# Kernel tuning notes

Hardware: AMD Instinct MI355X
Metric: run time of the kernel (lower is better)

The kernel has to match this reference:

```python
import jax, jax.numpy as jnp
import numpy as np

# Hyperparameters from init_kwargs
SIGMA = 0.01   # memristor conductance noise std
R = 1.0        # line resistance scale used in power accounting
WMAX1 = 1.0
WMAX2 = 1.0
B, C, H, W = 4, 3, 64, 64
K = 2                      # AvgPool2d kernel/stride
D1 = C * (H // K) * (W // K)   # 3072 flattened features after pooling
D2 = 2048
D3 = 1024


def setup_inputs() -> dict:
    key = jax.random.key(0)
    ks = jax.random.split(key, 4)
    x = jax.random.normal(ks[0], (B, C, H, W), jnp.float32)
    bias = jax.random.normal(ks[1], (C, H, W), jnp.float32) * 0.01
    W1 = jax.random.normal(ks[2], (D2, D1), jnp.float32) / np.float32(np.sqrt(D1))
    W2 = jax.random.normal(ks[3], (D3, D2), jnp.float32) / np.float32(np.sqrt(D2))
    g1 = jnp.float32(1.0)  # learnt_Gmax[0], initialized to Wmax[0]
    g2 = jnp.float32(1.0)  # learnt_Gmax[1]
    return {"x": x, "bias": bias, "W1": W1, "W2": W2, "g1": g1, "g2": g2}


def reference(x, bias, W1, W2, g1, g2):
    # input bias (MemSE.input_bias=True)
    x = x + bias[None]
    b = x.shape[0]
    eye2 = jnp.eye(D2, dtype=x.dtype)
    eye3 = jnp.eye(D3, dtype=x.dtype)

    # --- AvgPool2d(2,2): gamma is still empty at this point, only mean pooled ---
    x = x.reshape(b, C, H // K, K, W // K, K).mean(axis=(3, 5))
    x = x.reshape(b, -1)                        # [B, D1]

    # --- Linear 1: crossbar noise injection (gamma empty -> created here) ---
    c1 = g1 / WMAX1                             # conductance scaling G = c * W
    mu = x @ W1.T                               # [B, D2] mean propagation
    m2 = x * x                                  # E[x^2] (gamma == 0 before this layer)
    # two conductance arrays (pos/neg) each with iid noise var sigma^2, output /c
    vn1 = 2.0 * (SIGMA / c1) ** 2 * jnp.sum(m2, axis=-1)        # [B]
    gamma = vn1[:, None, None] * eye2[None]                      # [B, D2, D2]
    P_tot = (c1 / R) * jnp.einsum('oi,bi->b', jnp.abs(W1), m2)   # crossbar power

    # --- Softplus: first-order moment propagation (Jacobian = sigmoid(mu)) ---
    d = jax.nn.sigmoid(mu)                      # [B, D2]
    gamma = gamma * d[:, :, None] * d[:, None, :]
    mu = jax.nn.softplus(mu)

    # --- Linear 2: full covariance propagation W gamma W^T + noise diag ---
    c2 = g2 / WMAX2
    mu2 = mu @ W2.T                             # [B, D3]
    tmp = jnp.einsum('oi,bij->boj', W2, gamma)  # [B, D3, D2]
    gamma2 = jnp.einsum('boj,pj->bop', tmp, W2) # [B, D3, D3]
    m2b = mu * mu + jnp.diagonal(gamma, axis1=1, axis2=2)        # E[x^2]
    vn2 = 2.0 * (SIGMA / c2) ** 2 * jnp.sum(m2b, axis=-1)
    gamma2 = gamma2 + vn2[:, None, None] * eye3[None]
    P_tot = P_tot + (c2 / R) * jnp.einsum('oi,bi->b', jnp.abs(W2), m2b)

    return mu2, gamma2, P_tot
```

## Files before the change

### kernel.cpp

```cpp
#include <hip/hip_runtime.h>
#include <hip/hip_bf16.h>
#include <cstdint>

#define SIGMA 0.01f

constexpr int D1 = 3072;
constexpr int D2 = 2048;
constexpr int D3 = 1024;

typedef __bf16 bf16x8 __attribute__((ext_vector_type(8)));
typedef float f32x4 __attribute__((ext_vector_type(4)));

#define GLOAD16(gp, lp) \
  __builtin_amdgcn_global_load_lds((const __attribute__((address_space(1))) void*)(gp), \
                                   (__attribute__((address_space(3))) void*)(lp), 16, 0, 0)

__global__ void pool_kernel(const float* __restrict__ x, const float* __restrict__ bias,
                            float* __restrict__ pooled, float* __restrict__ Spart) {
  int idx = blockIdx.x * 256 + threadIdx.x;
  int b = idx / D1;
  int r = idx % D1;
  int c = r >> 10;
  int oh = (r >> 5) & 31;
  int ow = r & 31;
  int xb = ((b * 3 + c) * 64 + oh * 2) * 64 + ow * 2;
  int bb = (c * 64 + oh * 2) * 64 + ow * 2;
  float v = 0.25f * ((x[xb] + bias[bb]) + (x[xb + 1] + bias[bb + 1]) +
                     (x[xb + 64] + bias[bb + 64]) + (x[xb + 65] + bias[bb + 65]));
  pooled[idx] = v;
  float s = v * v;
  #pragma unroll
  for (int off = 32; off; off >>= 1) s += __shfl_down(s, off, 64);
  __shared__ float wsum[4];
  if ((threadIdx.x & 63) == 0) wsum[threadIdx.x >> 6] = s;
  __syncthreads();
  if (threadIdx.x == 0) Spart[blockIdx.x] = wsum[0] + wsum[1] + wsum[2] + wsum[3];
}

__global__ void lin1_kernel(const float* __restrict__ pooled, const float* __restrict__ W1,
                            const float* __restrict__ Spart, const float* __restrict__ g1p,
                            float* __restrict__ musp, float* __restrict__ dscale,
                            float* __restrict__ m2b, float* __restrict__ Pp1) {
  int o2 = blockIdx.x << 1, tid = threadIdx.x;
  const float4* w0p = (const float4*)(W1 + (size_t)o2 * D1);
  const float4* w1p = (const float4*)(W1 + (size_t)(o2 + 1) * D1);
  const float4* p4 = (const float4*)pooled;
  float a0[4] = {0,0,0,0}, q0[4] = {0,0,0,0}, a1[4] = {0,0,0,0}, q1[4] = {0,0,0,0};
  #pragma unroll
  for (int it = 0; it < 3; it++) {
    int i4 = tid + it * 256;
    float4 w0 = w0p[i4], w1 = w1p[i4];
    float x0x = fabsf(w0.x), x0y = fabsf(w0.y), x0z = fabsf(w0.z), x0w = fabsf(w0.w);
    float x1x = fabsf(w1.x), x1y = fabsf(w1.y), x1z = fabsf(w1.z), x1w = fabsf(w1.w);
    #pragma unroll
    for (int b = 0; b < 4; b++) {
      float4 p = p4[b * 768 + i4];
      float px = p.x * p.x, py = p.y * p.y, pz = p.z * p.z, pw = p.w * p.w;
      a0[b] += w0.x * p.x + w0.y * p.y + w0.z * p.z + w0.w * p.w;
      q0[b] += x0x * px + x0y * py + x0z * pz + x0w * pw;
      a1[b] += w1.x * p.x + w1.y * p.y + w1.z * p.z + w1.w * p.w;
      q1[b] += x1x * px + x1y * py + x1z * pz + x1w * pw;
    }
  }
  __shared__ float red[16][4];
  #pragma unroll
  for (int v = 0; v < 16; v++) {
    float s = (v < 4) ? a0[v] : (v < 8) ? q0[v - 4] : (v < 12) ? a1[v - 8] : q1[v - 12];
    #pragma unroll
    for (int off = 32; off; off >>= 1) s += __shfl_down(s, off, 64);
    if ((tid & 63) == 0) red[v][tid >> 6] = s;
  }
  __syncthreads();
  if (tid < 16) {
    float s = red[tid][0] + red[tid][1] + red[tid][2] + red[tid][3];
    int rr = tid >> 3, u = tid & 7;
    int o = o2 + rr;
    if (u < 4) {
      int b = u;
      float ss = 0.f;
      #pragma unroll
      for (int i = 0; i < 12; i++) ss += Spart[b * 12 + i];
      float c1 = g1p[0];
      float vn1 = 2.0f * (SIGMA / c1) * (SIGMA / c1) * ss;
      float d = 1.0f / (1.0f + expf(-s));
      float sp = fmaxf(s, 0.f) + log1pf(expf(-fabsf(s)));
      musp[b * D2 + o] = sp;
      dscale[b * D2 + o] = sqrtf(vn1) * d;
      m2b[b * D2 + o] = sp * sp + vn1 * d * d;
    } else {
      Pp1[(size_t)(u - 4) * D2 + o] = s;
    }
  }
}

__global__ void lin2_prep_kernel(const float* __restrict__ W2, const float* __restrict__ musp,
                                 const float* __restrict__ dscale, const float* __restrict__ m2b,
                                 __bf16* __restrict__ E, float* __restrict__ mu2,
                                 float* __restrict__ Pp2) {
  int o2 = blockIdx.x << 1, tid = threadIdx.x;
  int j0 = tid * 8;
  float w0[8], w1[8];
  *(float4*)&w0[0] = *(const float4*)(W2 + (size_t)o2 * D2 + j0);
  *(float4*)&w0[4] = *(const float4*)(W2 + (size_t)o2 * D2 + j0 + 4);
  *(float4*)&w1[0] = *(const float4*)(W2 + (size_t)(o2 + 1) * D2 + j0);
  *(float4*)&w1[4] = *(const float4*)(W2 + (size_t)(o2 + 1) * D2 + j0 + 4);
  float a0[4], q0[4], a1[4], q1[4];
  #pragma unroll
  for (int b = 0; b < 4; b++) {
    const float* ms = musp + b * D2 + j0;
    const float* dsc = dscale + b * D2 + j0;
    const float* mb = m2b + b * D2 + j0;
    bf16x8 e0, e1;
    float s0 = 0.f, p0 = 0.f, s1 = 0.f, p1 = 0.f;
    #pragma unroll
    for (int jj = 0; jj < 8; jj++) {
      float dv = dsc[jj], mv = ms[jj], bv = mb[jj];
      e0[jj] = (__bf16)(w0[jj] * dv);
      e1[jj] = (__bf16)(w1[jj] * dv);
      s0 += w0[jj] * mv;  p0 += fabsf(w0[jj]) * bv;
      s1 += w1[jj] * mv;  p1 += fabsf(w1[jj]) * bv;
    }
    *(bf16x8*)(E + ((size_t)b * D3 + o2) * D2 + j0) = e0;
    *(bf16x8*)(E + ((size_t)b * D3 + o2 + 1) * D2 + j0) = e1;
    a0[b] = s0; q0[b] = p0; a1[b] = s1; q1[b] = p1;
  }
  __shared__ float red[16][4];
  #pragma unroll
  for (int v = 0; v < 16; v++) {
    float s = (v < 4) ? a0[v] : (v < 8) ? q0[v - 4] : (v < 12) ? a1[v - 8] : q1[v - 12];
    #pragma unroll
    for (int off = 32; off; off >>= 1) s += __shfl_down(s, off, 64);
    if ((tid & 63) == 0) red[v][tid >> 6] = s;
  }
  __syncthreads();
  if (tid < 16) {
    float s = red[tid][0] + red[tid][1] + red[tid][2] + red[tid][3];
    int rr = tid >> 3, u = tid & 7;
    int o = o2 + rr;
    if (u < 4) mu2[u * D3 + o] = s;
    else Pp2[(size_t)(u - 4) * D3 + o] = s;
  }
}

__global__ void scalars_kernel(const float* __restrict__ m2b, const float* __restrict__ Pp1,
                               const float* __restrict__ Pp2, const float* __restrict__ g1p,
                               const float* __restrict__ g2p, float* __restrict__ vn2v,
                               float* __restrict__ Ptot) {
  int b = blockIdx.x, tid = threadIdx.x;
  float sm = 0.f, s1 = 0.f, s2 = 0.f;
  #pragma unroll
  for (int i = 0; i < 8; i++) {
    sm += m2b[(size_t)b * D2 + tid + i * 256];
    s1 += Pp1[(size_t)b * D2 + tid + i * 256];
  }
  #pragma unroll
  for (int i = 0; i < 4; i++) s2 += Pp2[(size_t)b * D3 + tid + i * 256];
  __shared__ float red[3][4];
  #pragma unroll
  for (int v = 0; v < 3; v++) {
    float s = (v == 0) ? sm : (v == 1) ? s1 : s2;
    #pragma unroll
    for (int off = 32; off; off >>= 1) s += __shfl_down(s, off, 64);
    if ((tid & 63) == 0) red[v][tid >> 6] = s;
  }
  __syncthreads();
  if (tid == 0) {
    float c2 = g2p[0];
    float smt = red[0][0] + red[0][1] + red[0][2] + red[0][3];
    float s1t = red[1][0] + red[1][1] + red[1][2] + red[1][3];
    float s2t = red[2][0] + red[2][1] + red[2][2] + red[2][3];
    vn2v[b] = 2.0f * (SIGMA / c2) * (SIGMA / c2) * smt;
    Ptot[b] = g1p[0] * s1t + c2 * s2t;
  }
}

__global__ __launch_bounds__(256, 4) void gamma2_gemm(const __bf16* __restrict__ E,
                                                      const float* __restrict__ vn2v,
                                                      float* __restrict__ gamma2) {
  int bid = blockIdx.x, tid = threadIdx.x;
  int wid = tid >> 6, lane = tid & 63;
  int wr = wid >> 1, wc = wid & 1;

  int xcd = bid & 7, r = bid >> 3;
  int b = xcd >> 1;
  int t = (r << 1) | (xcd & 1);
  int s = 135 - t;
  int k = (int)((sqrtf((float)(8 * s + 1)) - 1.0f) * 0.5f);
  while ((k + 1) * (k + 2) / 2 <= s) k++;
  while (k * (k + 1) / 2 > s) k--;
  int i = s - k * (k + 1) / 2;
  int tm = 15 - k, tn = 15 - i;

  __shared__ __bf16 As[2][4096], Bs[2][4096];
  char* AsB = (char*)As;
  char* BsB = (char*)Bs;

  const __bf16* Eb = E + (size_t)b * D3 * D2;
  int rb0 = wid >> 1, ks0 = wid & 1;
  int rb1 = (wid + 4) >> 1;
  int srow = lane >> 2, skc = lane & 3;
  const __bf16* gA0 = Eb + (size_t)(tm * 64 + rb0 * 16 + srow) * D2 + ks0 * 32 + skc * 8;
  const __bf16* gA1 = Eb + (size_t)(tm * 64 + rb1 * 16 + srow) * D2 + ks0 * 32 + skc * 8;
  const __bf16* gB0 = Eb + (size_t)(tn * 64 + rb0 * 16 + srow) * D2 + ks0 * 32 + skc * 8;
  const __bf16* gB1 = Eb + (size_t)(tn * 64 + rb1 * 16 + srow) * D2 + ks0 * 32 + skc * 8;
  unsigned dst0 = (unsigned)wid * 1024u;
  unsigned dst1 = dst0 + 4096u;

  int fr = lane & 15, kg = lane >> 4;
  unsigned po = (unsigned)(fr * 64 + kg * 16);
  unsigned aM0 = (unsigned)(wr * 4096) + po;
  unsigned aM1 = aM0 + 2048u;
  unsigned bN0 = (unsigned)(wc * 4096) + po;
  unsigned bN1 = bN0 + 2048u;

  f32x4 acc[2][2] = {};

#define STAGE(bufoff, kelem)                                   \
  {                                                            \
    GLOAD16(gA0 + (kelem), AsB + (bufoff) + dst0);             \
    GLOAD16(gA1 + (kelem), AsB + (bufoff) + dst1);             \
    GLOAD16(gB0 + (kelem), BsB + (bufoff) + dst0);             \
    GLOAD16(gB1 + (kelem), BsB + (bufoff) + dst1);             \
  }

#define COMPUTE(bufoff)                                                         \
  {                                                                             \
    _Pragma("unroll")                                                           \
    for (int ks2 = 0; ks2 < 2; ks2++) {                                         \
      unsigned kso = (unsigned)ks2 << 10;                                       \
      bf16x8 a0 = *(const bf16x8*)(AsB + (bufoff) + aM0 + kso);                 \
      bf16x8 a1 = *(const bf16x8*)(AsB + (bufoff) + aM1 + kso);                 \
      bf16x8 b0 = *(const bf16x8*)(BsB + (bufoff) + bN0 + kso);                 \
      bf16x8 b1 = *(const bf16x8*)(BsB + (bufoff) + bN1 + kso);                 \
      acc[0][0] = __builtin_amdgcn_mfma_f32_16x16x32_bf16(a0, b0, acc[0][0], 0, 0, 0); \
      acc[0][1] = __builtin_amdgcn_mfma_f32_16x16x32_bf16(a0, b1, acc[0][1], 0, 0, 0); \
      acc[1][0] = __builtin_amdgcn_mfma_f32_16x16x32_bf16(a1, b0, acc[1][0], 0, 0, 0); \
      acc[1][1] = __builtin_amdgcn_mfma_f32_16x16x32_bf16(a1, b1, acc[1][1], 0, 0, 0); \
    }                                                                           \
  }

  STAGE(0u, 0);
  __syncthreads();
  unsigned cur = 0;
  #pragma unroll 1
  for (int kt = 0; kt < 31; kt++) {
    unsigned nxt = cur ^ 8192u;
    STAGE(nxt, (kt + 1) * 64);
    COMPUTE(cur);
    __syncthreads();
    cur = nxt;
  }
  COMPUTE(cur);
#undef STAGE
#undef COMPUTE

  float vn2 = vn2v[b];
  float* outb = gamma2 + (size_t)b * D3 * D3;
  int row0 = tm * 64 + wr * 32 + kg * 4;
  int col0 = tn * 64 + wc * 32 + fr;
  #pragma unroll
  for (int mi = 0; mi < 2; mi++)
    #pragma unroll
    for (int ni = 0; ni < 2; ni++)
      #pragma unroll
      for (int rg = 0; rg < 4; rg++) {
        int row = row0 + mi * 16 + rg;
        int cc = col0 + ni * 16;
        float v = acc[mi][ni][rg];
        if (row == cc) v += vn2;
        outb[(size_t)row * D3 + cc] = v;
      }
  if (tm != tn) {
    #pragma unroll
    for (int mi = 0; mi < 2; mi++)
      #pragma unroll
      for (int ni = 0; ni < 2; ni++) {
        int cc = col0 + ni * 16;
        int rowb = row0 + mi * 16;
        *(f32x4*)(outb + (size_t)cc * D3 + rowb) = acc[mi][ni];
      }
  }
}

extern "C" void kernel_launch(void* const* d_in, const int* in_sizes, int n_in,
                              void* d_out, int out_size, void* d_ws, size_t ws_size,
                              hipStream_t stream) {
  (void)in_sizes; (void)n_in; (void)out_size; (void)ws_size;
  const float* x    = (const float*)d_in[0];
  const float* bias = (const float*)d_in[1];
  const float* W1   = (const float*)d_in[2];
  const float* W2   = (const float*)d_in[3];
  const float* g1   = (const float*)d_in[4];
  const float* g2   = (const float*)d_in[5];
  float* out = (float*)d_out;

  float* ws     = (float*)d_ws;
  float* pooled = ws;
  float* musp   = pooled + 4 * D1;
  float* dscale = musp + 4 * D2;
  float* m2b    = dscale + 4 * D2;
  float* Pp1    = m2b + 4 * D2;
  float* Pp2    = Pp1 + 4 * D2;
  float* Spart  = Pp2 + 4 * D3;
  float* vn2v   = Spart + 48;
  size_t used = (size_t)(4 * D1 + 4 * 4 * D2 + 4 * D3 + 64) * 4;
  size_t eoff = (used + 255) / 256 * 256;
  __bf16* E = (__bf16*)((char*)d_ws + eoff);

  float* mu2_out  = out;
  float* gam_out  = out + 4 * D3;
  float* ptot_out = out + 4 * D3 + (size_t)4 * D3 * D3;

  pool_kernel<<<48, 256, 0, stream>>>(x, bias, pooled, Spart);
  lin1_kernel<<<1024, 256, 0, stream>>>(pooled, W1, Spart, g1, musp, dscale, m2b, Pp1);
  lin2_prep_kernel<<<512, 256, 0, stream>>>(W2, musp, dscale, m2b, E, mu2_out, Pp2);
  scalars_kernel<<<4, 256, 0, stream>>>(m2b, Pp1, Pp2, g1, g2, vn2v, ptot_out);
  gamma2_gemm<<<544, 256, 0, stream>>>(E, vn2v, gam_out);
}
```

Before: 56.41 us.

## Fuse scalar reductions into gamma2 GEMM and deepen its LDS pipeline

Removes the separate scalars kernel launch. Each GEMM block now recomputes the per-batch vn2 sum itself, and the first four blocks compute P_tot. Separately, the GEMM's shared-memory staging grows from double to quad buffering, with explicit vmcnt waits and raw barriers so two tiles are in flight during compute. The trade-off is redundant m2b reads per block, and lower occupancy from the doubled LDS use and the launch bound dropping from 4 to 2 blocks.

After: 63.93 us. 1.13x slower.

```diff
diff --git a/kernel.cpp b/kernel.cpp
--- a/kernel.cpp
+++ b/kernel.cpp
@@ -142,41 +142,14 @@
   }
 }
 
-__global__ void scalars_kernel(const float* __restrict__ m2b, const float* __restrict__ Pp1,
-                               const float* __restrict__ Pp2, const float* __restrict__ g1p,
-                               const float* __restrict__ g2p, float* __restrict__ vn2v,
-                               float* __restrict__ Ptot) {
-  int b = blockIdx.x, tid = threadIdx.x;
-  float sm = 0.f, s1 = 0.f, s2 = 0.f;
-  #pragma unroll
-  for (int i = 0; i < 8; i++) {
-    sm += m2b[(size_t)b * D2 + tid + i * 256];
-    s1 += Pp1[(size_t)b * D2 + tid + i * 256];
-  }
-  #pragma unroll
-  for (int i = 0; i < 4; i++) s2 += Pp2[(size_t)b * D3 + tid + i * 256];
-  __shared__ float red[3][4];
-  #pragma unroll
-  for (int v = 0; v < 3; v++) {
-    float s = (v == 0) ? sm : (v == 1) ? s1 : s2;
-    #pragma unroll
-    for (int off = 32; off; off >>= 1) s += __shfl_down(s, off, 64);
-    if ((tid & 63) == 0) red[v][tid >> 6] = s;
-  }
-  __syncthreads();
-  if (tid == 0) {
-    float c2 = g2p[0];
-    float smt = red[0][0] + red[0][1] + red[0][2] + red[0][3];
-    float s1t = red[1][0] + red[1][1] + red[1][2] + red[1][3];
-    float s2t = red[2][0] + red[2][1] + red[2][2] + red[2][3];
-    vn2v[b] = 2.0f * (SIGMA / c2) * (SIGMA / c2) * smt;
-    Ptot[b] = g1p[0] * s1t + c2 * s2t;
-  }
-}
-
-__global__ __launch_bounds__(256, 4) void gamma2_gemm(const __bf16* __restrict__ E,
-                                                      const float* __restrict__ vn2v,
-                                                      float* __restrict__ gamma2) {
+__global__ __launch_bounds__(256, 2) void gamma2_gemm(const __bf16* __restrict__ E,
+                                                      const float* __restrict__ m2b,
+                                                      const float* __restrict__ Pp1,
+                                                      const float* __restrict__ Pp2,
+                                                      const float* __restrict__ g1p,
+                                                      const float* __restrict__ g2p,
+                                                      float* __restrict__ gamma2,
+                                                      float* __restrict__ Ptot) {
   int bid = blockIdx.x, tid = threadIdx.x;
   int wid = tid >> 6, lane = tid & 63;
   int wr = wid >> 1, wc = wid & 1;
@@ -191,7 +164,7 @@
   int i = s - k * (k + 1) / 2;
   int tm = 15 - k, tn = 15 - i;
 
-  __shared__ __bf16 As[2][4096], Bs[2][4096];
+  __shared__ __bf16 As[4][4096], Bs[4][4096];
   char* AsB = (char*)As;
   char* BsB = (char*)Bs;
 
@@ -240,21 +213,49 @@
   }
 
   STAGE(0u, 0);
-  __syncthreads();
-  unsigned cur = 0;
+  STAGE(8192u, 64);
   #pragma unroll 1
-  for (int kt = 0; kt < 31; kt++) {
-    unsigned nxt = cur ^ 8192u;
-    STAGE(nxt, (kt + 1) * 64);
-    COMPUTE(cur);
-    __syncthreads();
-    cur = nxt;
-  }
-  COMPUTE(cur);
+  for (int kt = 0; kt < 30; kt++) {
+    unsigned sb = (unsigned)((kt + 2) & 3) * 8192u;
+    STAGE(sb, (kt + 2) * 64);
+    asm volatile("s_waitcnt vmcnt(8)" ::: "memory");
+    __builtin_amdgcn_s_barrier();
+    __builtin_amdgcn_sched_barrier(0);
+    COMPUTE((unsigned)(kt & 3) * 8192u);
+  }
+  asm volatile("s_waitcnt vmcnt(4)" ::: "memory");
+  __builtin_amdgcn_s_barrier();
+  __builtin_amdgcn_sched_barrier(0);
+  COMPUTE((unsigned)(30 & 3) * 8192u);
+  asm volatile("s_waitcnt vmcnt(0)" ::: "memory");
+  __builtin_amdgcn_s_barrier();
+  __builtin_amdgcn_sched_barrier(0);
+  COMPUTE((unsigned)(31 & 3) * 8192u);
 #undef STAGE
 #undef COMPUTE
 
-  float vn2 = vn2v[b];
+  float c2 = g2p[0];
+  float sm = 0.f;
+  #pragma unroll
+  for (int ii = 0; ii < 32; ii++) sm += m2b[(size_t)b * D2 + lane + ii * 64];
+  #pragma unroll
+  for (int off = 32; off; off >>= 1) sm += __shfl_xor(sm, off, 64);
+  float vn2 = 2.0f * (SIGMA / c2) * (SIGMA / c2) * sm;
+
+  if (bid < 4 && wid == 0) {
+    float s1 = 0.f, s2 = 0.f;
+    #pragma unroll
+    for (int ii = 0; ii < 32; ii++) s1 += Pp1[(size_t)bid * D2 + lane + ii * 64];
+    #pragma unroll
+    for (int ii = 0; ii < 16; ii++) s2 += Pp2[(size_t)bid * D3 + lane + ii * 64];
+    #pragma unroll
+    for (int off = 32; off; off >>= 1) {
+      s1 += __shfl_down(s1, off, 64);
+      s2 += __shfl_down(s2, off, 64);
+    }
+    if (lane == 0) Ptot[bid] = g1p[0] * s1 + c2 * s2;
+  }
+
   float* outb = gamma2 + (size_t)b * D3 * D3;
   int row0 = tm * 64 + wr * 32 + kg * 4;
   int col0 = tn * 64 + wc * 32 + fr;
@@ -302,7 +303,6 @@
   float* Pp1    = m2b + 4 * D2;
   float* Pp2    = Pp1 + 4 * D2;
   float* Spart  = Pp2 + 4 * D3;
-  float* vn2v   = Spart + 48;
   size_t used = (size_t)(4 * D1 + 4 * 4 * D2 + 4 * D3 + 64) * 4;
   size_t eoff = (used + 255) / 256 * 256;
   __bf16* E = (__bf16*)((char*)d_ws + eoff);
@@ -314,6 +314,5 @@
   pool_kernel<<<48, 256, 0, stream>>>(x, bias, pooled, Spart);
   lin1_kernel<<<1024, 256, 0, stream>>>(pooled, W1, Spart, g1, musp, dscale, m2b, Pp1);
   lin2_prep_kernel<<<512, 256, 0, stream>>>(W2, musp, dscale, m2b, E, mu2_out, Pp2);
-  scalars_kernel<<<4, 256, 0, stream>>>(m2b, Pp1, Pp2, g1, g2, vn2v, ptot_out);
-  gamma2_gemm<<<544, 256, 0, stream>>>(E, vn2v, gam_out);
-}
+  gamma2_gemm<<<544, 256, 0, stream>>>(E, m2b, Pp1, Pp2, g1, g2, gam_out, ptot_out);
+}
```

## Fuse pooling into linear-1, fold scalar reductions into later kernels

Applied to the files above, without the earlier changes.

Moves the pooling into the first linear kernel: every block recomputes the full pooled input (all batches) into shared memory, then handles four output rows instead of two. The vn2 reduction becomes four extra blocks of the lin2 prep kernel, and the power total is reduced inside the gamma2 GEMM, so two launches disappear. The cost is redundant pooling work and a 48KB shared-memory buffer per block in lin1, which limits occupancy and adds input reads in exchange for fewer launches.

Result: slower. 60.56 us (+7.4%).

```diff
diff --git a/kernel.cpp b/kernel.cpp
--- a/kernel.cpp
+++ b/kernel.cpp
@@ -15,73 +15,90 @@
   __builtin_amdgcn_global_load_lds((const __attribute__((address_space(1))) void*)(gp), \
                                    (__attribute__((address_space(3))) void*)(lp), 16, 0, 0)
 
-__global__ void pool_kernel(const float* __restrict__ x, const float* __restrict__ bias,
-                            float* __restrict__ pooled, float* __restrict__ Spart) {
-  int idx = blockIdx.x * 256 + threadIdx.x;
-  int b = idx / D1;
-  int r = idx % D1;
-  int c = r >> 10;
-  int oh = (r >> 5) & 31;
-  int ow = r & 31;
-  int xb = ((b * 3 + c) * 64 + oh * 2) * 64 + ow * 2;
-  int bb = (c * 64 + oh * 2) * 64 + ow * 2;
-  float v = 0.25f * ((x[xb] + bias[bb]) + (x[xb + 1] + bias[bb + 1]) +
-                     (x[xb + 64] + bias[bb + 64]) + (x[xb + 65] + bias[bb + 65]));
-  pooled[idx] = v;
-  float s = v * v;
-  #pragma unroll
-  for (int off = 32; off; off >>= 1) s += __shfl_down(s, off, 64);
-  __shared__ float wsum[4];
-  if ((threadIdx.x & 63) == 0) wsum[threadIdx.x >> 6] = s;
-  __syncthreads();
-  if (threadIdx.x == 0) Spart[blockIdx.x] = wsum[0] + wsum[1] + wsum[2] + wsum[3];
-}
-
-__global__ void lin1_kernel(const float* __restrict__ pooled, const float* __restrict__ W1,
-                            const float* __restrict__ Spart, const float* __restrict__ g1p,
-                            float* __restrict__ musp, float* __restrict__ dscale,
-                            float* __restrict__ m2b, float* __restrict__ Pp1) {
-  int o2 = blockIdx.x << 1, tid = threadIdx.x;
-  const float4* w0p = (const float4*)(W1 + (size_t)o2 * D1);
-  const float4* w1p = (const float4*)(W1 + (size_t)(o2 + 1) * D1);
-  const float4* p4 = (const float4*)pooled;
-  float a0[4] = {0,0,0,0}, q0[4] = {0,0,0,0}, a1[4] = {0,0,0,0}, q1[4] = {0,0,0,0};
+__global__ __launch_bounds__(256) void lin1_fused(const float* __restrict__ x,
+                                                  const float* __restrict__ bias,
+                                                  const float* __restrict__ W1,
+                                                  const float* __restrict__ g1p,
+                                                  float* __restrict__ musp,
+                                                  float* __restrict__ dscale,
+                                                  float* __restrict__ m2b,
+                                                  float* __restrict__ Pp1) {
+  __shared__ float pooled_s[12288];
+  __shared__ float sred[4][4];
+  __shared__ float Ssum_s[4];
+  __shared__ float red[32][4];
+  int tid = threadIdx.x;
+
+  float sacc[4] = {0, 0, 0, 0};
+  #pragma unroll
+  for (int it = 0; it < 24; it++) {
+    int b = it / 6;
+    int lp = (it % 6) * 256 + tid;
+    int r = lp * 2;
+    int c = r >> 10, oh = (r >> 5) & 31, ow = r & 31;
+    int xb = ((b * 3 + c) * 64 + oh * 2) * 64 + ow * 2;
+    int bb = (c * 64 + oh * 2) * 64 + ow * 2;
+    float4 x0 = *(const float4*)(x + xb);
+    float4 x1 = *(const float4*)(x + xb + 64);
+    float4 b0 = *(const float4*)(bias + bb);
+    float4 b1 = *(const float4*)(bias + bb + 64);
+    float v0 = 0.25f * ((x0.x + b0.x) + (x0.y + b0.y) + (x1.x + b1.x) + (x1.y + b1.y));
+    float v1 = 0.25f * ((x0.z + b0.z) + (x0.w + b0.w) + (x1.z + b1.z) + (x1.w + b1.w));
+    *(float2*)(pooled_s + b * 3072 + r) = make_float2(v0, v1);
+    sacc[b] += v0 * v0 + v1 * v1;
+  }
+  #pragma unroll
+  for (int v = 0; v < 4; v++) {
+    float sv = sacc[v];
+    #pragma unroll
+    for (int off = 32; off; off >>= 1) sv += __shfl_down(sv, off, 64);
+    if ((tid & 63) == 0) sred[v][tid >> 6] = sv;
+  }
+  __syncthreads();
+  if (tid < 4) Ssum_s[tid] = sred[tid][0] + sred[tid][1] + sred[tid][2] + sred[tid][3];
+  __syncthreads();
+
+  int o4 = blockIdx.x << 2;
+  const float4* w0p = (const float4*)(W1 + (size_t)(o4 + 0) * D1);
+  const float4* w1p = (const float4*)(W1 + (size_t)(o4 + 1) * D1);
+  const float4* w2p = (const float4*)(W1 + (size_t)(o4 + 2) * D1);
+  const float4* w3p = (const float4*)(W1 + (size_t)(o4 + 3) * D1);
+  const float4* p4 = (const float4*)pooled_s;
+  float a[4][4] = {}, q[4][4] = {};
   #pragma unroll
   for (int it = 0; it < 3; it++) {
     int i4 = tid + it * 256;
-    float4 w0 = w0p[i4], w1 = w1p[i4];
-    float x0x = fabsf(w0.x), x0y = fabsf(w0.y), x0z = fabsf(w0.z), x0w = fabsf(w0.w);
-    float x1x = fabsf(w1.x), x1y = fabsf(w1.y), x1z = fabsf(w1.z), x1w = fabsf(w1.w);
+    float4 w[4];
+    w[0] = w0p[i4]; w[1] = w1p[i4]; w[2] = w2p[i4]; w[3] = w3p[i4];
     #pragma unroll
     for (int b = 0; b < 4; b++) {
       float4 p = p4[b * 768 + i4];
       float px = p.x * p.x, py = p.y * p.y, pz = p.z * p.z, pw = p.w * p.w;
-      a0[b] += w0.x * p.x + w0.y * p.y + w0.z * p.z + w0.w * p.w;
-      q0[b] += x0x * px + x0y * py + x0z * pz + x0w * pw;
-      a1[b] += w1.x * p.x + w1.y * p.y + w1.z * p.z + w1.w * p.w;
-      q1[b] += x1x * px + x1y * py + x1z * pz + x1w * pw;
-    }
-  }
-  __shared__ float red[16][4];
-  #pragma unroll
-  for (int v = 0; v < 16; v++) {
-    float s = (v < 4) ? a0[v] : (v < 8) ? q0[v - 4] : (v < 12) ? a1[v - 8] : q1[v - 12];
+      #pragma unroll
+      for (int rr = 0; rr < 4; rr++) {
+        a[rr][b] += w[rr].x * p.x + w[rr].y * p.y + w[rr].z * p.z + w[rr].w * p.w;
+        q[rr][b] += fabsf(w[rr].x) * px + fabsf(w[rr].y) * py +
+                    fabsf(w[rr].z) * pz + fabsf(w[rr].w) * pw;
+      }
+    }
+  }
+  #pragma unroll
+  for (int v = 0; v < 32; v++) {
+    float s = (v < 16) ? a[v >> 2][v & 3] : q[(v - 16) >> 2][(v - 16) & 3];
     #pragma unroll
     for (int off = 32; off; off >>= 1) s += __shfl_down(s, off, 64);
     if ((tid & 63) == 0) red[v][tid >> 6] = s;
   }
   __syncthreads();
-  if (tid < 16) {
-    float s = red[tid][0] + red[tid][1] + red[tid][2] + red[tid][3];
+  if (tid < 32) {
     int rr = tid >> 3, u = tid & 7;
-    int o = o2 + rr;
+    int idx = (u < 4) ? (rr * 4 + u) : (16 + rr * 4 + (u - 4));
+    float s = red[idx][0] + red[idx][1] + red[idx][2] + red[idx][3];
+    int o = o4 + rr;
     if (u < 4) {
       int b = u;
-      float ss = 0.f;
-      #pragma unroll
-      for (int i = 0; i < 12; i++) ss += Spart[b * 12 + i];
       float c1 = g1p[0];
-      float vn1 = 2.0f * (SIGMA / c1) * (SIGMA / c1) * ss;
+      float vn1 = 2.0f * (SIGMA / c1) * (SIGMA / c1) * Ssum_s[b];
       float d = 1.0f / (1.0f + expf(-s));
       float sp = fmaxf(s, 0.f) + log1pf(expf(-fabsf(s)));
       musp[b * D2 + o] = sp;
@@ -95,9 +112,27 @@
 
 __global__ void lin2_prep_kernel(const float* __restrict__ W2, const float* __restrict__ musp,
                                  const float* __restrict__ dscale, const float* __restrict__ m2b,
-                                 __bf16* __restrict__ E, float* __restrict__ mu2,
-                                 float* __restrict__ Pp2) {
-  int o2 = blockIdx.x << 1, tid = threadIdx.x;
+                                 const float* __restrict__ g2p, __bf16* __restrict__ E,
+                                 float* __restrict__ mu2, float* __restrict__ Pp2,
+                                 float* __restrict__ vn2v) {
+  int tid = threadIdx.x;
+  if (blockIdx.x >= 512) {
+    int b = blockIdx.x - 512;
+    float sm = 0.f;
+    #pragma unroll
+    for (int i = 0; i < 8; i++) sm += m2b[(size_t)b * D2 + tid + i * 256];
+    #pragma unroll
+    for (int off = 32; off; off >>= 1) sm += __shfl_down(sm, off, 64);
+    __shared__ float red1[4];
+    if ((tid & 63) == 0) red1[tid >> 6] = sm;
+    __syncthreads();
+    if (tid == 0) {
+      float c2 = g2p[0];
+      vn2v[b] = 2.0f * (SIGMA / c2) * (SIGMA / c2) * (red1[0] + red1[1] + red1[2] + red1[3]);
+    }
+    return;
+  }
+  int o2 = blockIdx.x << 1;
   int j0 = tid * 8;
   float w0[8], w1[8];
   *(float4*)&w0[0] = *(const float4*)(W2 + (size_t)o2 * D2 + j0);
@@ -142,41 +177,14 @@
   }
 }
 
-__global__ void scalars_kernel(const float* __restrict__ m2b, const float* __restrict__ Pp1,
-                               const float* __restrict__ Pp2, const float* __restrict__ g1p,
-                               const float* __restrict__ g2p, float* __restrict__ vn2v,
-                               float* __restrict__ Ptot) {
-  int b = blockIdx.x, tid = threadIdx.x;
-  float sm = 0.f, s1 = 0.f, s2 = 0.f;
-  #pragma unroll
-  for (int i = 0; i < 8; i++) {
-    sm += m2b[(size_t)b * D2 + tid + i * 256];
-    s1 += Pp1[(size_t)b * D2 + tid + i * 256];
-  }
-  #pragma unroll
-  for (int i = 0; i < 4; i++) s2 += Pp2[(size_t)b * D3 + tid + i * 256];
-  __shared__ float red[3][4];
-  #pragma unroll
-  for (int v = 0; v < 3; v++) {
-    float s = (v == 0) ? sm : (v == 1) ? s1 : s2;
-    #pragma unroll
-    for (int off = 32; off; off >>= 1) s += __shfl_down(s, off, 64);
-    if ((tid & 63) == 0) red[v][tid >> 6] = s;
-  }
-  __syncthreads();
-  if (tid == 0) {
-    float c2 = g2p[0];
-    float smt = red[0][0] + red[0][1] + red[0][2] + red[0][3];
-    float s1t = red[1][0] + red[1][1] + red[1][2] + red[1][3];
-    float s2t = red[2][0] + red[2][1] + red[2][2] + red[2][3];
-    vn2v[b] = 2.0f * (SIGMA / c2) * (SIGMA / c2) * smt;
-    Ptot[b] = g1p[0] * s1t + c2 * s2t;
-  }
-}
-
 __global__ __launch_bounds__(256, 4) void gamma2_gemm(const __bf16* __restrict__ E,
                                                       const float* __restrict__ vn2v,
-                                                      float* __restrict__ gamma2) {
+                                                      const float* __restrict__ Pp1,
+                                                      const float* __restrict__ Pp2,
+                                                      const float* __restrict__ g1p,
+                                                      const float* __restrict__ g2p,
+                                                      float* __restrict__ gamma2,
+                                                      float* __restrict__ Ptot) {
   int bid = blockIdx.x, tid = threadIdx.x;
   int wid = tid >> 6, lane = tid & 63;
   int wr = wid >> 1, wc = wid & 1;
@@ -254,6 +262,21 @@
 #undef STAGE
 #undef COMPUTE
 
+  float c2 = g2p[0];
+  if (bid < 4 && wid == 0) {
+    float s1 = 0.f, s2 = 0.f;
+    #pragma unroll
+    for (int ii = 0; ii < 32; ii++) s1 += Pp1[(size_t)bid * D2 + lane + ii * 64];
+    #pragma unroll
+    for (int ii = 0; ii < 16; ii++) s2 += Pp2[(size_t)bid * D3 + lane + ii * 64];
+    #pragma unroll
+    for (int off = 32; off; off >>= 1) {
+      s1 += __shfl_down(s1, off, 64);
+      s2 += __shfl_down(s2, off, 64);
+    }
+    if (lane == 0) Ptot[bid] = g1p[0] * s1 + c2 * s2;
+  }
+
   float vn2 = vn2v[b];
   float* outb = gamma2 + (size_t)b * D3 * D3;
   int row0 = tm * 64 + wr * 32 + kg * 4;
@@ -295,15 +318,13 @@
   float* out = (float*)d_out;
 
   float* ws     = (float*)d_ws;
-  float* pooled = ws;
-  float* musp   = pooled + 4 * D1;
+  float* musp   = ws;
   float* dscale = musp + 4 * D2;
   float* m2b    = dscale + 4 * D2;
   float* Pp1    = m2b + 4 * D2;
   float* Pp2    = Pp1 + 4 * D2;
-  float* Spart  = Pp2 + 4 * D3;
-  float* vn2v   = Spart + 48;
-  size_t used = (size_t)(4 * D1 + 4 * 4 * D2 + 4 * D3 + 64) * 4;
+  float* vn2v   = Pp2 + 4 * D3;
+  size_t used = (size_t)(4 * 4 * D2 + 4 * D3 + 16) * 4;
   size_t eoff = (used + 255) / 256 * 256;
   __bf16* E = (__bf16*)((char*)d_ws + eoff);
 
@@ -311,9 +332,7 @@
   float* gam_out  = out + 4 * D3;
   float* ptot_out = out + 4 * D3 + (size_t)4 * D3 * D3;
 
-  pool_kernel<<<48, 256, 0, stream>>>(x, bias, pooled, Spart);
-  lin1_kernel<<<1024, 256, 0, stream>>>(pooled, W1, Spart, g1, musp, dscale, m2b, Pp1);
-  lin2_prep_kernel<<<512, 256, 0, stream>>>(W2, musp, dscale, m2b, E, mu2_out, Pp2);
-  scalars_kernel<<<4, 256, 0, stream>>>(m2b, Pp1, Pp2, g1, g2, vn2v, ptot_out);
-  gamma2_gemm<<<544, 256, 0, stream>>>(E, vn2v, gam_out);
+  lin1_fused<<<512, 256, 0, stream>>>(x, bias, W1, g1, musp, dscale, m2b, Pp1);
+  lin2_prep_kernel<<<516, 256, 0, stream>>>(W2, musp, dscale, m2b, g2, E, mu2_out, Pp2, vn2v);
+  gamma2_gemm<<<544, 256, 0, stream>>>(E, vn2v, Pp1, Pp2, g1, g2, gam_out, ptot_out);
 }
```
